# Optimization experiments

Hardware: AMD Instinct MI355X
Metric: run time of the kernel (lower is better)

Reference implementation:

```python
import jax, jax.numpy as jnp
import numpy as np

B, S, D_IN, D_OUT, H = 4, 2048, 1024, 1024, 16
HD = D_OUT // H  # head_dim = 64


def setup_inputs() -> dict:
    key = jax.random.key(0)
    ks = jax.random.split(key, 9)
    sc_in = 1.0 / np.sqrt(D_IN)
    sc_out = 1.0 / np.sqrt(D_OUT)
    return {
        "x": jax.random.normal(ks[0], (B, S, D_IN), dtype=jnp.float32),
        "Wq": jax.random.normal(ks[1], (D_IN, D_OUT), dtype=jnp.float32) * sc_in,
        "bq": jax.random.normal(ks[2], (D_OUT,), dtype=jnp.float32) * 0.01,
        "Wk": jax.random.normal(ks[3], (D_IN, D_OUT), dtype=jnp.float32) * sc_in,
        "bk": jax.random.normal(ks[4], (D_OUT,), dtype=jnp.float32) * 0.01,
        "Wv": jax.random.normal(ks[5], (D_IN, D_OUT), dtype=jnp.float32) * sc_in,
        "bv": jax.random.normal(ks[6], (D_OUT,), dtype=jnp.float32) * 0.01,
        "Wo": jax.random.normal(ks[7], (D_OUT, D_OUT), dtype=jnp.float32) * sc_out,
        "bo": jax.random.normal(ks[8], (D_OUT,), dtype=jnp.float32) * 0.01,
    }


def reference(x, Wq, bq, Wk, bk, Wv, bv, Wo, bo):
    b, s, _ = x.shape
    # QKV projections -> [b, h, s, hd]
    def proj(W, bias):
        return (x @ W + bias).reshape(b, s, H, HD).transpose(0, 2, 1, 3)
    q, k, v = proj(Wq, bq), proj(Wk, bk), proj(Wv, bv)
    # scaled scores [b, h, s, s] with causal mask (future positions -> -inf)
    scores = jnp.einsum("bhqd,bhkd->bhqk", q, k) / jnp.sqrt(jnp.float32(HD))
    causal = jnp.triu(jnp.ones((s, s), dtype=bool), k=1)
    scores = jnp.where(causal, -jnp.inf, scores)
    attn = jax.nn.softmax(scores, axis=-1)  # dropout p=0.0 -> identity
    ctx = jnp.einsum("bhqk,bhkd->bhqd", attn, v)
    ctx = ctx.transpose(0, 2, 1, 3).reshape(b, s, D_OUT)
    return ctx @ Wo + bo
```

## Files before the change

kernel.cpp:

```cpp
#include <hip/hip_runtime.h>
#include <hip/hip_bf16.h>

#define B_   4
#define S_   2048
#define H_   16
#define HD_  64
#define D_   1024
#define M_   (B_ * S_)
#define N3_  3072

typedef unsigned short u16;
typedef __bf16 bf16x8 __attribute__((ext_vector_type(8)));
typedef float  f32x4  __attribute__((ext_vector_type(4)));
typedef int    i32x4  __attribute__((ext_vector_type(4)));
typedef unsigned short u16x8 __attribute__((ext_vector_type(8)));
typedef unsigned short u16x4 __attribute__((ext_vector_type(4)));

__device__ __forceinline__ float b2f(u16 u) {
    unsigned int x = ((unsigned int)u) << 16;
    return __builtin_bit_cast(float, x);
}
__device__ __forceinline__ u16 f2b(float f) {
    unsigned int x = __builtin_bit_cast(unsigned int, f);
    x += 0x7fffu + ((x >> 16) & 1u);
    return (u16)(x >> 16);
}

typedef const __attribute__((address_space(1))) unsigned int* gas_u32p;
typedef __attribute__((address_space(3))) unsigned int* las_u32p;
__device__ __forceinline__ void gl_lds16(const u16* g, u16* lds_base) {
    __builtin_amdgcn_global_load_lds((gas_u32p)g, (las_u32p)lds_base, 16, 0, 0);
}

__global__ __launch_bounds__(256) void cvt_k(const float* __restrict__ in,
                                             u16* __restrict__ out) {
    size_t i = ((size_t)blockIdx.x * 256 + threadIdx.x) * 8;
    float4 a = *(const float4*)(in + i);
    float4 b = *(const float4*)(in + i + 4);
    *(u16x8*)(out + i) = u16x8{f2b(a.x), f2b(a.y), f2b(a.z), f2b(a.w),
                               f2b(b.x), f2b(b.y), f2b(b.z), f2b(b.w)};
}

__global__ __launch_bounds__(256) void transpose4_k(
    const float* __restrict__ w0, const float* __restrict__ w1,
    const float* __restrict__ w2, const float* __restrict__ w3,
    u16* __restrict__ oqkv, u16* __restrict__ owo, float scale0) {
    __shared__ u16 t[32][33];
    const int z = blockIdx.z;
    const float* in = (z == 0) ? w0 : (z == 1) ? w1 : (z == 2) ? w2 : w3;
    u16* out = (z < 3) ? oqkv + (size_t)z * D_ * D_ : owo;
    const float sc = (z == 0) ? scale0 : 1.0f;
    const int x0 = blockIdx.x * 32, y0 = blockIdx.y * 32;
    const int tx = threadIdx.x & 31, ty = threadIdx.x >> 5;
#pragma unroll
    for (int i = 0; i < 32; i += 8)
        t[ty + i][tx] = f2b(in[(size_t)(y0 + ty + i) * D_ + x0 + tx] * sc);
    __syncthreads();
#pragma unroll
    for (int i = 0; i < 32; i += 8)
        out[(size_t)(x0 + ty + i) * D_ + y0 + tx] = t[tx][ty + i];
}

#define QBM 256
#define QBN 192
#define QBK 64

__global__ __launch_bounds__(512, 2) void gemm_qkv256(
    const u16* __restrict__ A, const u16* __restrict__ Bt,
    const float* __restrict__ b0, const float* __restrict__ b1,
    const float* __restrict__ b2, float cscale,
    u16* __restrict__ Qo, u16* __restrict__ Ko, u16* __restrict__ Vto,
    int M, int N, int K)
{
    __shared__ __align__(16) u16 As[2][QBM * QBK];
    __shared__ __align__(16) u16 Bs[2][QBN * QBK];

    const int tid  = threadIdx.x;
    const int lane = tid & 63;
    const int wave = tid >> 6;
    const int wr = wave >> 2, wc = wave & 3;
    const int l15 = lane & 15, quad = lane >> 4, s7 = l15 & 7;
    const int r8  = lane >> 3;
    const int csw = ((lane & 7) ^ r8) * 8;
    const int m0 = blockIdx.x * QBM, n0 = blockIdx.y * QBN;
    (void)M; (void)N;

    const u16* Ag = A  + (size_t)(m0 + wave * 8 + r8) * K + csw;
    const u16* Bg = Bt + (size_t)(n0 + wave * 8 + r8) * K + csw;
    u16* AsW = &As[0][0] + wave * 8 * QBK;
    u16* BsW = &Bs[0][0] + wave * 8 * QBK;
    const size_t rowK64 = (size_t)64 * K;

    auto stgA = [&](int buf, int u, int kt) {
        gl_lds16(Ag + (size_t)u * rowK64 + kt * QBK,
                 AsW + buf * (QBM * QBK) + u * 64 * QBK);
    };
    auto stgB = [&](int buf, int u, int kt) {
        gl_lds16(Bg + (size_t)u * rowK64 + kt * QBK,
                 BsW + buf * (QBN * QBK) + u * 64 * QBK);
    };

    f32x4 acc[8][3] = {};

    stgA(0, 0, 0); stgA(0, 1, 0); stgA(0, 2, 0); stgA(0, 3, 0);
    stgB(0, 0, 0); stgB(0, 1, 0); stgB(0, 2, 0);
    stgB(1, 0, 1); stgB(1, 1, 1); stgB(1, 2, 1);
    asm volatile("s_waitcnt vmcnt(3)" ::: "memory");
    __builtin_amdgcn_s_barrier();

    const int NIT = K / (2 * QBK);
    for (int it = 0; it < NIT; ++it) {
        const bool last = (it == NIT - 1);
        const int t1 = 2 * it + 1, t2 = 2 * it + 2, t3 = 2 * it + 3;
        bf16x8 bn[3][2];
#pragma unroll
        for (int ph = 0; ph < 4; ++ph) {
            const int hb = ph >> 1;
            const int qg = ph & 1;
            const u16* as = &As[hb][0];
            const u16* bs = &Bs[hb][0];
            if (qg == 0) {
#pragma unroll
                for (int n = 0; n < 3; ++n) {
                    const u16* bp = bs + (wc * 48 + n * 16 + l15) * QBK;
                    bn[n][0] = *(const bf16x8*)(bp + ((quad    ) ^ s7) * 8);
                    bn[n][1] = *(const bf16x8*)(bp + ((quad + 4) ^ s7) * 8);
                }
            }
            bf16x8 af[4][2];
#pragma unroll
            for (int r = 0; r < 4; ++r) {
                const u16* ap = as + (wr * 128 + (qg * 4 + r) * 16 + l15) * QBK;
                af[r][0] = *(const bf16x8*)(ap + ((quad    ) ^ s7) * 8);
                af[r][1] = *(const bf16x8*)(ap + ((quad + 4) ^ s7) * 8);
            }
            if (ph == 0) { stgA(1, 0, t1); stgA(1, 1, t1);
                           stgA(1, 2, t1); stgA(1, 3, t1); }
            if (!last) {
                if (ph == 1) { stgB(0, 0, t2); stgB(0, 1, t2); stgB(0, 2, t2); }
                if (ph == 2) { stgA(0, 0, t2); stgA(0, 1, t2);
                               stgA(0, 2, t2); stgA(0, 3, t2); }
                if (ph == 3) { stgB(1, 0, t3); stgB(1, 1, t3); stgB(1, 2, t3); }
            }
            __builtin_amdgcn_s_barrier();
            asm volatile("s_waitcnt lgkmcnt(0)" ::: "memory");
            __builtin_amdgcn_sched_barrier(0);
            __builtin_amdgcn_s_setprio(1);
#pragma unroll
            for (int r = 0; r < 4; ++r)
#pragma unroll
                for (int n = 0; n < 3; ++n) {
                    acc[qg * 4 + r][n] = __builtin_amdgcn_mfma_f32_16x16x32_bf16(
                        af[r][0], bn[n][0], acc[qg * 4 + r][n], 0, 0, 0);
                    acc[qg * 4 + r][n] = __builtin_amdgcn_mfma_f32_16x16x32_bf16(
                        af[r][1], bn[n][1], acc[qg * 4 + r][n], 0, 0, 0);
                }
            __builtin_amdgcn_s_setprio(0);
            if (ph == 1) {
                if (!last) asm volatile("s_waitcnt vmcnt(3)" ::: "memory");
                else       asm volatile("s_waitcnt vmcnt(0)" ::: "memory");
            }
            if (ph == 3 && !last)
                asm volatile("s_waitcnt vmcnt(3)" ::: "memory");
            __builtin_amdgcn_s_barrier();
        }
    }

    int qidxv[3]; int ncolv[3]; float bvv[3];
#pragma unroll
    for (int nt = 0; nt < 3; ++nt) {
        const int col = n0 + wc * 48 + nt * 16 + l15;
        qidxv[nt] = col >> 10;
        ncolv[nt] = col & (D_ - 1);
        bvv[nt] = (qidxv[nt] == 0) ? b0[ncolv[nt]] * cscale
                : (qidxv[nt] == 1) ? b1[ncolv[nt]] : b2[ncolv[nt]];
    }
#pragma unroll
    for (int mt = 0; mt < 8; ++mt) {
        const int rbase = m0 + wr * 128 + mt * 16 + quad * 4;
#pragma unroll
        for (int r2 = 0; r2 < 4; ++r2) {
#pragma unroll
            for (int nt = 0; nt < 3; ++nt) {
                if (qidxv[nt] == 2) continue;
                u16* dst = (qidxv[nt] == 0) ? Qo : Ko;
                dst[(size_t)(rbase + r2) * D_ + ncolv[nt]] =
                    f2b(acc[mt][nt][r2] + bvv[nt]);
            }
        }
#pragma unroll
        for (int nt = 0; nt < 3; ++nt) {
            if (qidxv[nt] != 2) continue;
            const int bidx = rbase >> 11, s = rbase & (S_ - 1);
            const int hh = ncolv[nt] >> 6, hd = ncolv[nt] & 63;
            u16x4 pk{f2b(acc[mt][nt][0] + bvv[nt]), f2b(acc[mt][nt][1] + bvv[nt]),
                     f2b(acc[mt][nt][2] + bvv[nt]), f2b(acc[mt][nt][3] + bvv[nt])};
            *(u16x4*)(Vto + (((size_t)(bidx * H_ + hh)) * HD_ + hd) * S_ + s) = pk;
        }
    }
}

#define BM 128
#define BN 128
#define BK 64

template <int MODE>
__global__ __launch_bounds__(256) void gemm_core(
    const u16* __restrict__ A, const u16* __restrict__ Bt,
    const float* __restrict__ b0, const float* __restrict__ b1,
    const float* __restrict__ b2, float cscale,
    void* __restrict__ O0, void* __restrict__ O1, void* __restrict__ O2,
    int M, int N, int K)
{
    __shared__ __align__(16) u16 As[BM * BK];
    __shared__ __align__(16) u16 Bs[BN * BK];

    const int tid  = threadIdx.x;
    const int lane = tid & 63;
    const int wave = tid >> 6;
    const int wr = wave >> 1, wc = wave & 1;
    const int l15 = lane & 15, quad = lane >> 4;
    const int m0 = blockIdx.x * BM, n0 = blockIdx.y * BN;
    const int r8 = lane >> 3;
    const int csw = ((lane & 7) ^ r8) * 8;

    f32x4 acc[4][4] = {};

    for (int k0 = 0; k0 < K; k0 += BK) {
#pragma unroll
        for (int i = 0; i < 4; ++i) {
            const int row = wave * 32 + i * 8 + r8;
            gl_lds16(A  + (size_t)(m0 + row) * K + k0 + csw,
                     As + (wave * 32 + i * 8) * BK);
            gl_lds16(Bt + (size_t)(n0 + row) * K + k0 + csw,
                     Bs + (wave * 32 + i * 8) * BK);
        }
        __syncthreads();
        bf16x8 af[4][2], bfr[4][2];
#pragma unroll
        for (int t = 0; t < 4; ++t) {
            const u16* ap = As + (wr * 64 + t * 16 + l15) * BK;
            const u16* bp = Bs + (wc * 64 + t * 16 + l15) * BK;
            const int s7 = l15 & 7;
            af[t][0]  = *(const bf16x8*)(ap + ((quad    ) ^ s7) * 8);
            af[t][1]  = *(const bf16x8*)(ap + ((quad + 4) ^ s7) * 8);
            bfr[t][0] = *(const bf16x8*)(bp + ((quad    ) ^ s7) * 8);
            bfr[t][1] = *(const bf16x8*)(bp + ((quad + 4) ^ s7) * 8);
        }
#pragma unroll
        for (int mt = 0; mt < 4; ++mt)
#pragma unroll
            for (int nt = 0; nt < 4; ++nt) {
                acc[mt][nt] = __builtin_amdgcn_mfma_f32_16x16x32_bf16(
                    af[mt][0], bfr[nt][0], acc[mt][nt], 0, 0, 0);
                acc[mt][nt] = __builtin_amdgcn_mfma_f32_16x16x32_bf16(
                    af[mt][1], bfr[nt][1], acc[mt][nt], 0, 0, 0);
            }
        __syncthreads();
    }

#pragma unroll
    for (int nt = 0; nt < 4; ++nt) {
        const int col = n0 + wc * 64 + nt * 16 + l15;
        if constexpr (MODE == 1) {
            const float bv = b0[col];
#pragma unroll
            for (int mt = 0; mt < 4; ++mt) {
                const int rbase = m0 + wr * 64 + mt * 16 + quad * 4;
#pragma unroll
                for (int r2 = 0; r2 < 4; ++r2)
                    ((float*)O0)[(size_t)(rbase + r2) * N + col] =
                        acc[mt][nt][r2] + bv;
            }
        } else {
            const int qidx = col >> 10, ncol = col & (D_ - 1);
            const float bv = (qidx == 0) ? b0[ncol] * cscale
                           : (qidx == 1) ? b1[ncol] : b2[ncol];
#pragma unroll
            for (int mt = 0; mt < 4; ++mt) {
                const int rbase = m0 + wr * 64 + mt * 16 + quad * 4;
                if (qidx == 2) {
                    const int bidx = rbase >> 11, s = rbase & (S_ - 1);
                    const int hh = ncol >> 6, hd = ncol & 63;
                    u16x4 pk{f2b(acc[mt][nt][0] + bv), f2b(acc[mt][nt][1] + bv),
                             f2b(acc[mt][nt][2] + bv), f2b(acc[mt][nt][3] + bv)};
                    *(u16x4*)((u16*)O2 +
                        (((size_t)(bidx * H_ + hh)) * HD_ + hd) * S_ + s) = pk;
                } else {
                    u16* dst = (qidx == 0) ? (u16*)O0 : (u16*)O1;
#pragma unroll
                    for (int r2 = 0; r2 < 4; ++r2)
                        dst[(size_t)(rbase + r2) * D_ + ncol] =
                            f2b(acc[mt][nt][r2] + bv);
                }
            }
        }
    }
}

__global__ __launch_bounds__(256, 4) void attn_mfma_k(
    const u16* __restrict__ Qm, const u16* __restrict__ Km,
    const u16* __restrict__ Vtg, u16* __restrict__ Om)
{
    __shared__ __align__(16) u16 Kbuf[2][64 * 64];
    __shared__ __align__(16) u16 Vbuf[2][64 * 64];
    __shared__ __align__(16) u16 Ps[4][16 * 64];

    const int tid  = threadIdx.x;
    const int lane = tid & 63;
    const int wave = tid >> 6;
    const int l15  = lane & 15;
    const int quad = lane >> 4;
    const int s7   = l15 & 7;
    const int bh = blockIdx.x, b = bh >> 4, h = bh & (H_ - 1);
    const int j  = blockIdx.y;
    const int dg0 = j, dg1 = 31 - j;

    const u16* Qg = Qm + (size_t)b * S_ * D_ + h * HD_;
    const u16* Kg = Km + (size_t)b * S_ * D_ + h * HD_;
    const u16* Vg = Vtg + ((size_t)(b * H_ + h)) * HD_ * S_;

    bf16x8 qf0[2], qf1[2];
    {
        const u16* qp = Qg + (size_t)(dg0 * 64 + wave * 16 + l15) * D_ + quad * 8;
        qf0[0] = *(const bf16x8*)qp; qf0[1] = *(const bf16x8*)(qp + 32);
        qp = Qg + (size_t)(dg1 * 64 + wave * 16 + l15) * D_ + quad * 8;
        qf1[0] = *(const bf16x8*)qp; qf1[1] = *(const bf16x8*)(qp + 32);
    }

    f32x4 of0[4] = {}, of1[4] = {};
    float lacc0 = 0.f, lacc1 = 0.f;
    const int qloc = wave * 16 + l15;
    const int r8 = lane >> 3;
    const int csw = ((lane & 7) ^ r8) * 8;
    const int srcA = l15 + ((quad & 1) << 5);
    const int srcB = srcA + 16;

    auto stage = [&](int t, int bsel) {
        u16* kb = Kbuf[bsel];
        u16* vb = Vbuf[bsel];
#pragma unroll
        for (int i = 0; i < 2; ++i) {
            const int row = wave * 16 + i * 8 + r8;
            gl_lds16(Kg + (size_t)(t * 64 + row) * D_ + csw,
                     kb + (wave * 16 + i * 8) * 64);
            gl_lds16(Vg + (size_t)row * S_ + t * 64 + csw,
                     vb + (wave * 16 + i * 8) * 64);
        }
    };

    auto smax = [&](const f32x4 (&sf)[4], bool domask, float& la,
                    bf16x8& pfa, bf16x8& pfb) {
        unsigned int w[4][2];
        float ls = 0.f;
        if (domask) {
#pragma unroll
            for (int kt = 0; kt < 4; ++kt)
#pragma unroll
                for (int hh = 0; hh < 2; ++hh) {
                    float v0 = sf[kt][2 * hh], v1 = sf[kt][2 * hh + 1];
                    if (kt * 16 + quad * 4 + 2 * hh     > qloc) v0 = -INFINITY;
                    if (kt * 16 + quad * 4 + 2 * hh + 1 > qloc) v1 = -INFINITY;
                    float p0 = __builtin_amdgcn_exp2f(v0);
                    float p1 = __builtin_amdgcn_exp2f(v1);
                    ls += p0 + p1;
                    w[kt][hh] = (__builtin_bit_cast(unsigned int, p0) >> 16) |
                                (__builtin_bit_cast(unsigned int, p1) & 0xFFFF0000u);
                }
        } else {
#pragma unroll
            for (int kt = 0; kt < 4; ++kt)
#pragma unroll
                for (int hh = 0; hh < 2; ++hh) {
                    float p0 = __builtin_amdgcn_exp2f(sf[kt][2 * hh]);
                    float p1 = __builtin_amdgcn_exp2f(sf[kt][2 * hh + 1]);
                    ls += p0 + p1;
                    w[kt][hh] = (__builtin_bit_cast(unsigned int, p0) >> 16) |
                                (__builtin_bit_cast(unsigned int, p1) & 0xFFFF0000u);
                }
        }
        la += ls;
        const bool hi = (quad & 2) != 0;
        i32x4 f0, f1;
        {
            int a0, a1;
            a0 = __shfl((int)w[0][0], srcA); a1 = __shfl((int)w[1][0], srcA);
            f0.x = hi ? a1 : a0;
            a0 = __shfl((int)w[0][1], srcA); a1 = __shfl((int)w[1][1], srcA);
            f0.y = hi ? a1 : a0;
            a0 = __shfl((int)w[0][0], srcB); a1 = __shfl((int)w[1][0], srcB);
            f0.z = hi ? a1 : a0;
            a0 = __shfl((int)w[0][1], srcB); a1 = __shfl((int)w[1][1], srcB);
            f0.w = hi ? a1 : a0;
            a0 = __shfl((int)w[2][0], srcA); a1 = __shfl((int)w[3][0], srcA);
            f1.x = hi ? a1 : a0;
            a0 = __shfl((int)w[2][1], srcA); a1 = __shfl((int)w[3][1], srcA);
            f1.y = hi ? a1 : a0;
            a0 = __shfl((int)w[2][0], srcB); a1 = __shfl((int)w[3][0], srcB);
            f1.z = hi ? a1 : a0;
            a0 = __shfl((int)w[2][1], srcB); a1 = __shfl((int)w[3][1], srcB);
            f1.w = hi ? a1 : a0;
        }
        pfa = __builtin_bit_cast(bf16x8, f0);
        pfb = __builtin_bit_cast(bf16x8, f1);
    };

    const int T = 32 - j;
    stage(0, 0);
    for (int t = 0; t < T; ++t) {
        __syncthreads();
        if (t + 1 < T) stage(t + 1, (t + 1) & 1);
        const u16* kb = Kbuf[t & 1];
        const u16* vb = Vbuf[t & 1];

        if (t <= dg0) {
            f32x4 s0[4], s1[4];
            __builtin_amdgcn_s_setprio(1);
#pragma unroll
            for (int kt = 0; kt < 4; ++kt) {
                const u16* kp = kb + (kt * 16 + l15) * 64;
                bf16x8 k0 = *(const bf16x8*)(kp + ((quad    ) ^ s7) * 8);
                bf16x8 k1 = *(const bf16x8*)(kp + ((quad + 4) ^ s7) * 8);
                f32x4 a = {};
                a = __builtin_amdgcn_mfma_f32_16x16x32_bf16(k0, qf0[0], a, 0, 0, 0);
                a = __builtin_amdgcn_mfma_f32_16x16x32_bf16(k1, qf0[1], a, 0, 0, 0);
                s0[kt] = a;
                f32x4 c = {};
                c = __builtin_amdgcn_mfma_f32_16x16x32_bf16(k0, qf1[0], c, 0, 0, 0);
                c = __builtin_amdgcn_mfma_f32_16x16x32_bf16(k1, qf1[1], c, 0, 0, 0);
                s1[kt] = c;
            }
            __builtin_amdgcn_s_setprio(0);
            bf16x8 p00, p01, p10, p11;
            smax(s0, t == dg0, lacc0, p00, p01);
            smax(s1, false,    lacc1, p10, p11);
            __builtin_amdgcn_s_setprio(1);
#pragma unroll
            for (int dt = 0; dt < 4; ++dt) {
                const u16* vp = vb + (dt * 16 + l15) * 64;
                bf16x8 v0 = *(const bf16x8*)(vp + ((quad    ) ^ s7) * 8);
                bf16x8 v1 = *(const bf16x8*)(vp + ((quad + 4) ^ s7) * 8);
                of0[dt] = __builtin_amdgcn_mfma_f32_16x16x32_bf16(v0, p00, of0[dt], 0, 0, 0);
                of0[dt] = __builtin_amdgcn_mfma_f32_16x16x32_bf16(v1, p01, of0[dt], 0, 0, 0);
                of1[dt] = __builtin_amdgcn_mfma_f32_16x16x32_bf16(v0, p10, of1[dt], 0, 0, 0);
                of1[dt] = __builtin_amdgcn_mfma_f32_16x16x32_bf16(v1, p11, of1[dt], 0, 0, 0);
            }
            __builtin_amdgcn_s_setprio(0);
        } else {
            f32x4 s1[4];
            __builtin_amdgcn_s_setprio(1);
#pragma unroll
            for (int kt = 0; kt < 4; ++kt) {
                const u16* kp = kb + (kt * 16 + l15) * 64;
                bf16x8 k0 = *(const bf16x8*)(kp + ((quad    ) ^ s7) * 8);
                bf16x8 k1 = *(const bf16x8*)(kp + ((quad + 4) ^ s7) * 8);
                f32x4 c = {};
                c = __builtin_amdgcn_mfma_f32_16x16x32_bf16(k0, qf1[0], c, 0, 0, 0);
                c = __builtin_amdgcn_mfma_f32_16x16x32_bf16(k1, qf1[1], c, 0, 0, 0);
                s1[kt] = c;
            }
            __builtin_amdgcn_s_setprio(0);
            bf16x8 p10, p11;
            smax(s1, t == dg1, lacc1, p10, p11);
            __builtin_amdgcn_s_setprio(1);
#pragma unroll
            for (int dt = 0; dt < 4; ++dt) {
                const u16* vp = vb + (dt * 16 + l15) * 64;
                bf16x8 v0 = *(const bf16x8*)(vp + ((quad    ) ^ s7) * 8);
                bf16x8 v1 = *(const bf16x8*)(vp + ((quad + 4) ^ s7) * 8);
                of1[dt] = __builtin_amdgcn_mfma_f32_16x16x32_bf16(v0, p10, of1[dt], 0, 0, 0);
                of1[dt] = __builtin_amdgcn_mfma_f32_16x16x32_bf16(v1, p11, of1[dt], 0, 0, 0);
            }
            __builtin_amdgcn_s_setprio(0);
        }
    }

    u16* pw = Ps[wave];
    auto epi = [&](const f32x4 (&o)[4], float la, int dgq) {
        float ls = la;
        ls += __shfl_xor(ls, 16);
        ls += __shfl_xor(ls, 32);
        const float inv = 1.f / ls;
#pragma unroll
        for (int dt = 0; dt < 4; ++dt) {
            const int g = dt * 16 + quad * 4;
            const int pos = ((g >> 3) ^ s7) * 8 + (g & 7);
            *(u16x4*)(pw + l15 * 64 + pos) =
                u16x4{f2b(o[dt][0] * inv), f2b(o[dt][1] * inv),
                      f2b(o[dt][2] * inv), f2b(o[dt][3] * inv)};
        }
        const int r  = lane >> 2;
        const int cp = lane & 3;
        u16x8 o0 = *(const u16x8*)(pw + r * 64 + ((2 * cp    ) ^ (r & 7)) * 8);
        u16x8 o1 = *(const u16x8*)(pw + r * 64 + ((2 * cp + 1) ^ (r & 7)) * 8);
        u16* op = Om + ((size_t)(b * S_ + dgq * 64 + wave * 16 + r)) * D_ + h * 64 + cp * 16;
        *(u16x8*)op = o0;
        *(u16x8*)(op + 8) = o1;
    };
    epi(of0, lacc0, dg0);
    epi(of1, lacc1, dg1);
}

extern "C" void kernel_launch(void* const* d_in, const int* in_sizes, int n_in,
                              void* d_out, int out_size, void* d_ws, size_t ws_size,
                              hipStream_t stream)
{
    (void)in_sizes; (void)n_in; (void)out_size; (void)ws_size;
    const float* x  = (const float*)d_in[0];
    const float* Wq = (const float*)d_in[1];
    const float* bq = (const float*)d_in[2];
    const float* Wk = (const float*)d_in[3];
    const float* bk = (const float*)d_in[4];
    const float* Wv = (const float*)d_in[5];
    const float* bv = (const float*)d_in[6];
    const float* Wo = (const float*)d_in[7];
    const float* bo = (const float*)d_in[8];

    const float cscale = 0.18033688011112042f;

    u16* ws = (u16*)d_ws;
    const size_t MD = (size_t)M_ * D_;
    const size_t DD = (size_t)D_ * D_;
    u16* xb    = ws;
    u16* Qb    = xb + MD;
    u16* Kb    = Qb + MD;
    u16* Vtb   = Kb + MD;
    u16* Cb    = Vtb + MD;
    u16* WqkvT = Cb + MD;
    u16* WoT   = WqkvT + 3 * DD;

    cvt_k<<<M_ * D_ / 2048, 256, 0, stream>>>(x, xb);

    transpose4_k<<<dim3(D_ / 32, D_ / 32, 4), 256, 0, stream>>>(
        Wq, Wk, Wv, Wo, WqkvT, WoT, cscale);

    gemm_qkv256<<<dim3(M_ / QBM, N3_ / QBN), 512, 0, stream>>>(
        xb, WqkvT, bq, bk, bv, cscale, Qb, Kb, Vtb, M_, N3_, D_);

    attn_mfma_k<<<dim3(B_ * H_, 16), 256, 0, stream>>>(Qb, Kb, Vtb, Cb);

    gemm_core<1><<<dim3(M_ / BM, D_ / BN), 256, 0, stream>>>(
        Cb, WoT, bo, nullptr, nullptr, 1.0f, d_out, nullptr, nullptr, M_, D_, D_);
}
```

Measured before the change: 284.3 us.

## Use permlane swaps for P transpose, reuse K buffer for epilogue, drop setprio

```diff
diff --git a/kernel.cpp b/kernel.cpp
--- a/kernel.cpp
+++ b/kernel.cpp
@@ -13,6 +13,7 @@
 typedef __bf16 bf16x8 __attribute__((ext_vector_type(8)));
 typedef float  f32x4  __attribute__((ext_vector_type(4)));
 typedef int    i32x4  __attribute__((ext_vector_type(4)));
+typedef unsigned int u32x2 __attribute__((ext_vector_type(2)));
 typedef unsigned short u16x8 __attribute__((ext_vector_type(8)));
 typedef unsigned short u16x4 __attribute__((ext_vector_type(4)));
 
@@ -298,13 +299,13 @@
     }
 }
 
-__global__ __launch_bounds__(256, 4) void attn_mfma_k(
+__global__ __launch_bounds__(256)
+__attribute__((amdgpu_waves_per_eu(4, 4))) void attn_mfma_k(
     const u16* __restrict__ Qm, const u16* __restrict__ Km,
     const u16* __restrict__ Vtg, u16* __restrict__ Om)
 {
     __shared__ __align__(16) u16 Kbuf[2][64 * 64];
     __shared__ __align__(16) u16 Vbuf[2][64 * 64];
-    __shared__ __align__(16) u16 Ps[4][16 * 64];
 
     const int tid  = threadIdx.x;
     const int lane = tid & 63;
@@ -333,8 +334,6 @@
     const int qloc = wave * 16 + l15;
     const int r8 = lane >> 3;
     const int csw = ((lane & 7) ^ r8) * 8;
-    const int srcA = l15 + ((quad & 1) << 5);
-    const int srcB = srcA + 16;
 
     auto stage = [&](int t, int bsel) {
         u16* kb = Kbuf[bsel];
@@ -380,26 +379,21 @@
                 }
         }
         la += ls;
-        const bool hi = (quad & 2) != 0;
         i32x4 f0, f1;
         {
-            int a0, a1;
-            a0 = __shfl((int)w[0][0], srcA); a1 = __shfl((int)w[1][0], srcA);
-            f0.x = hi ? a1 : a0;
-            a0 = __shfl((int)w[0][1], srcA); a1 = __shfl((int)w[1][1], srcA);
-            f0.y = hi ? a1 : a0;
-            a0 = __shfl((int)w[0][0], srcB); a1 = __shfl((int)w[1][0], srcB);
-            f0.z = hi ? a1 : a0;
-            a0 = __shfl((int)w[0][1], srcB); a1 = __shfl((int)w[1][1], srcB);
-            f0.w = hi ? a1 : a0;
-            a0 = __shfl((int)w[2][0], srcA); a1 = __shfl((int)w[3][0], srcA);
-            f1.x = hi ? a1 : a0;
-            a0 = __shfl((int)w[2][1], srcA); a1 = __shfl((int)w[3][1], srcA);
-            f1.y = hi ? a1 : a0;
-            a0 = __shfl((int)w[2][0], srcB); a1 = __shfl((int)w[3][0], srcB);
-            f1.z = hi ? a1 : a0;
-            a0 = __shfl((int)w[2][1], srcB); a1 = __shfl((int)w[3][1], srcB);
-            f1.w = hi ? a1 : a0;
+            u32x2 t, r;
+            t = __builtin_amdgcn_permlane32_swap(w[0][0], w[1][0], false, false);
+            r = __builtin_amdgcn_permlane16_swap(t[0], t[1], false, false);
+            f0.x = (int)r[0]; f0.z = (int)r[1];
+            t = __builtin_amdgcn_permlane32_swap(w[0][1], w[1][1], false, false);
+            r = __builtin_amdgcn_permlane16_swap(t[0], t[1], false, false);
+            f0.y = (int)r[0]; f0.w = (int)r[1];
+            t = __builtin_amdgcn_permlane32_swap(w[2][0], w[3][0], false, false);
+            r = __builtin_amdgcn_permlane16_swap(t[0], t[1], false, false);
+            f1.x = (int)r[0]; f1.z = (int)r[1];
+            t = __builtin_amdgcn_permlane32_swap(w[2][1], w[3][1], false, false);
+            r = __builtin_amdgcn_permlane16_swap(t[0], t[1], false, false);
+            f1.y = (int)r[0]; f1.w = (int)r[1];
         }
         pfa = __builtin_bit_cast(bf16x8, f0);
         pfb = __builtin_bit_cast(bf16x8, f1);
@@ -415,7 +409,6 @@
 
         if (t <= dg0) {
             f32x4 s0[4], s1[4];
-            __builtin_amdgcn_s_setprio(1);
 #pragma unroll
             for (int kt = 0; kt < 4; ++kt) {
                 const u16* kp = kb + (kt * 16 + l15) * 64;
@@ -430,11 +423,9 @@
                 c = __builtin_amdgcn_mfma_f32_16x16x32_bf16(k1, qf1[1], c, 0, 0, 0);
                 s1[kt] = c;
             }
-            __builtin_amdgcn_s_setprio(0);
             bf16x8 p00, p01, p10, p11;
             smax(s0, t == dg0, lacc0, p00, p01);
             smax(s1, false,    lacc1, p10, p11);
-            __builtin_amdgcn_s_setprio(1);
 #pragma unroll
             for (int dt = 0; dt < 4; ++dt) {
                 const u16* vp = vb + (dt * 16 + l15) * 64;
@@ -445,10 +436,8 @@
                 of1[dt] = __builtin_amdgcn_mfma_f32_16x16x32_bf16(v0, p10, of1[dt], 0, 0, 0);
                 of1[dt] = __builtin_amdgcn_mfma_f32_16x16x32_bf16(v1, p11, of1[dt], 0, 0, 0);
             }
-            __builtin_amdgcn_s_setprio(0);
         } else {
             f32x4 s1[4];
-            __builtin_amdgcn_s_setprio(1);
 #pragma unroll
             for (int kt = 0; kt < 4; ++kt) {
                 const u16* kp = kb + (kt * 16 + l15) * 64;
@@ -459,10 +448,8 @@
                 c = __builtin_amdgcn_mfma_f32_16x16x32_bf16(k1, qf1[1], c, 0, 0, 0);
                 s1[kt] = c;
             }
-            __builtin_amdgcn_s_setprio(0);
             bf16x8 p10, p11;
             smax(s1, t == dg1, lacc1, p10, p11);
-            __builtin_amdgcn_s_setprio(1);
 #pragma unroll
             for (int dt = 0; dt < 4; ++dt) {
                 const u16* vp = vb + (dt * 16 + l15) * 64;
@@ -471,11 +458,11 @@
                 of1[dt] = __builtin_amdgcn_mfma_f32_16x16x32_bf16(v0, p10, of1[dt], 0, 0, 0);
                 of1[dt] = __builtin_amdgcn_mfma_f32_16x16x32_bf16(v1, p11, of1[dt], 0, 0, 0);
             }
-            __builtin_amdgcn_s_setprio(0);
-        }
-    }
-
-    u16* pw = Ps[wave];
+        }
+    }
+
+    __syncthreads();
+    u16* pw = &Kbuf[0][0] + wave * 16 * 64;
     auto epi = [&](const f32x4 (&o)[4], float la, int dgq) {
         float ls = la;
         ls += __shfl_xor(ls, 16);
```

Measured after the change: 266.4 us. 1.07x faster.
